# Performance work log

Hardware: AMD Instinct MI355X
Metric: run time of the kernel (lower is better)

The kernel has to match this reference:

```python
import jax, jax.numpy as jnp
import numpy as np

VOCAB_FACTORS = (16, 16, 16, 8)   # prod = 32768 = vocab_size
DIM_FACTORS = (4, 4, 4, 4)        # prod = 256   = projection_dim
RANKS = (1, 16, 16, 16, 1)        # tt_rank = 16
NUM_CORES = 4


def _core_shapes():
    return [(RANKS[k], VOCAB_FACTORS[k], DIM_FACTORS[k], RANKS[k + 1])
            for k in range(NUM_CORES)]


def _vocab_strides():
    # big-endian mixed-radix decomposition of a flat vocab index
    strides = []
    s = 1
    for n in reversed(VOCAB_FACTORS):
        strides.append(s)
        s *= n
    return tuple(reversed(strides))


def tt_lookup(cores, idx):
    """Reconstruct embedding rows from TT cores.
    cores[k]: [r_k, n_k, m_k, r_{k+1}];  idx: int array [...].
    Returns [..., prod(m_k)]."""
    flat = idx.reshape(-1)                                # [Bf]
    res = jnp.ones((flat.shape[0], 1, 1), dtype=cores[0].dtype)  # [Bf, M=1, r=1]
    for core, n, st in zip(cores, VOCAB_FACTORS, _vocab_strides()):
        digit = (flat // st) % n                          # [Bf]
        g = jnp.moveaxis(core[:, digit], 1, 0)            # [Bf, r, m, r']
        res = jnp.einsum('bMr,brms->bMms', res, g)        # [Bf, M, m, r']
        res = res.reshape(res.shape[0], -1, res.shape[-1])  # [Bf, M*m, r']
    D = res.shape[1]
    return res[..., 0].reshape(idx.shape + (D,))


def setup_inputs() -> dict:
    key = jax.random.key(0)
    ks = jax.random.split(key, 12)
    B, NEG, V = 8192, 20, int(np.prod(VOCAB_FACTORS))
    inp = {
        'center_words': jax.random.randint(ks[0], (B, 1), 0, V),
        'target_words': jax.random.randint(ks[1], (B, 1), 0, V),
        'negative_words': jax.random.randint(ks[2], (B, NEG), 0, V),
    }
    # embedding_v: glorot-style init spread over cores
    for k, shp in enumerate(_core_shapes()):
        glorot_std = float(np.sqrt(2.0 / (shp[0] * shp[1] + shp[2] * shp[3])))
        inp[f'v_core{k}'] = glorot_std * jax.random.normal(ks[3 + k], shp, dtype=jnp.float32)
    # embedding_u: stddev=1e-4 per the module
    for k, shp in enumerate(_core_shapes()):
        inp[f'u_core{k}'] = 1e-4 * jax.random.normal(ks[7 + k], shp, dtype=jnp.float32)
    return inp


def reference(center_words, target_words, negative_words,
              v_core0, v_core1, v_core2, v_core3,
              u_core0, u_core1, u_core2, u_core3):
    v_cores = (v_core0, v_core1, v_core2, v_core3)
    u_cores = (u_core0, u_core1, u_core2, u_core3)
    center_embeds = tt_lookup(v_cores, center_words)      # [B, 1, D]
    target_embeds = tt_lookup(u_cores, target_words)      # [B, 1, D]
    neg_embeds = -tt_lookup(u_cores, negative_words)      # [B, K, D]
    # target.bmm(center^T).squeeze(2) -> [B, 1]
    positive_score = jnp.einsum('bsd,btd->bs', target_embeds, center_embeds)
    # sum over negatives then view [B, 1]
    negative_score = jnp.sum(
        jnp.einsum('bkd,btd->bk', neg_embeds, center_embeds),
        axis=1, keepdims=True)                            # [B, 1]
    loss = jax.nn.log_sigmoid(positive_score) + jax.nn.log_sigmoid(negative_score)
    return -jnp.mean(loss)
```

## Files before the change

### kernel.cpp

```cpp
#include <hip/hip_runtime.h>
#include <hip/hip_bf16.h>

#define DEVINL __device__ __forceinline__

constexpr int NNEG   = 20;
constexpr int NBATCH = 8192;

constexpr int OFF_CORES = 0;
constexpr int N_CORE_ELEMS = 68608;
constexpr int OFF_H01V = 68608;
constexpr int OFF_H23V = 134144;
constexpr int OFF_H01U = 166912;
constexpr int OFF_H23U = 232448;
constexpr int OFF_PART = 265216;
constexpr int OFF_UTAB_F = 267264;
constexpr size_t WS_NEED_BYTES = (size_t)OFF_UTAB_F * 4 + (size_t)32768 * 256 * 2;

constexpr int CO_V0 = 0,     CO_V1 = 1024,  CO_V2 = 17408, CO_V3 = 33792;
constexpr int CO_U0 = 34304, CO_U1 = 35328, CO_U2 = 51712, CO_U3 = 68096;

DEVINL float bfbits_to_f32(unsigned short h) {
  unsigned int u = ((unsigned int)h) << 16;
  float f;
  __builtin_memcpy(&f, &u, sizeof(f));
  return f;
}

DEVINL unsigned short f32_to_bfbits(float f) {
  __hip_bfloat16 h = __float2bfloat16(f);
  unsigned short hb;
  __builtin_memcpy(&hb, &h, 2);
  return hb;
}

DEVINL bool sniff_is_f32(const void* probe) {
  const unsigned short* p = (const unsigned short*)probe;
  int insane = 0;
#pragma unroll 1
  for (int i = 0; i < 64; ++i) {
    unsigned short h = p[i];
    int e = (h >> 7) & 0xFF;
    if (h != 0 && (e < 90 || e > 140)) insane++;
  }
  return insane > 8;
}

__global__ void tt_convert(const void* v0, const void* v1, const void* v2, const void* v3,
                           const void* u0, const void* u1, const void* u2, const void* u3,
                           float* __restrict__ ws) {
  int t = blockIdx.x * 256 + threadIdx.x;
  if (t >= N_CORE_ELEMS) return;
  bool isF32 = sniff_is_f32(v1);
  const void* src;
  int local;
  if      (t < CO_V1) { src = v0; local = t; }
  else if (t < CO_V2) { src = v1; local = t - CO_V1; }
  else if (t < CO_V3) { src = v2; local = t - CO_V2; }
  else if (t < CO_U0) { src = v3; local = t - CO_V3; }
  else if (t < CO_U1) { src = u0; local = t - CO_U0; }
  else if (t < CO_U2) { src = u1; local = t - CO_U1; }
  else if (t < CO_U3) { src = u2; local = t - CO_U2; }
  else                { src = u3; local = t - CO_U3; }
  float val = isF32 ? ((const float*)src)[local]
                    : bfbits_to_f32(((const unsigned short*)src)[local]);
  ws[t] = val;
}

__global__ void tt_htables(float* __restrict__ ws) {
  int t = blockIdx.x * 256 + threadIdx.x;
  const float* cores = ws + OFF_CORES;
  bool isU = t >= 98304;
  int lt = isU ? t - 98304 : t;
  const float* c0 = cores + (isU ? CO_U0 : CO_V0);
  const float* c1 = cores + (isU ? CO_U1 : CO_V1);
  const float* c2 = cores + (isU ? CO_U2 : CO_V2);
  const float* c3 = cores + (isU ? CO_U3 : CO_V3);
  float* dst = ws + (isU ? OFF_H01U : OFF_H01V);

  if (lt < 65536) {
    int combo = lt >> 8, e = lt & 255;
    int d0 = combo >> 4, d1 = combo & 15;
    int M01 = e >> 4, r2 = e & 15;
    int m0 = M01 >> 2, m1 = M01 & 3;
    float s = 0.f;
#pragma unroll
    for (int r1 = 0; r1 < 16; ++r1)
      s = fmaf(c0[(d0 * 4 + m0) * 16 + r1], c1[((r1 * 16 + d1) * 4 + m1) * 16 + r2], s);
    dst[lt] = s;
  } else {
    int lt2 = lt - 65536;
    int combo = lt2 >> 8, e = lt2 & 255;
    int d2 = combo >> 3, d3 = combo & 7;
    int m23 = e >> 4, r2 = e & 15;
    int m2 = m23 >> 2, m3 = m23 & 3;
    float s = 0.f;
#pragma unroll
    for (int r3 = 0; r3 < 16; ++r3)
      s = fmaf(c2[((r2 * 16 + d2) * 4 + m2) * 16 + r3], c3[(r3 * 8 + d3) * 4 + m3], s);
    dst[65536 + lt2] = s;
  }
}

DEVINL float4 ld4(const float* p) { return *reinterpret_cast<const float4*>(p); }

DEVINL float logsigf(float x) {
  return fminf(x, 0.0f) - log1pf(expf(-fabsf(x)));
}

DEVINL void frag16(const float* __restrict__ A, const float* __restrict__ Bt,
                   int l, float e[4]) {
  const float* Ar = A + (l >> 2) * 16;
  const float* Br = Bt + (l & 3) * 64;
  float a[16], b[64];
#pragma unroll
  for (int i = 0; i < 4; ++i) *reinterpret_cast<float4*>(&a[4 * i]) = ld4(Ar + 4 * i);
#pragma unroll
  for (int i = 0; i < 16; ++i) *reinterpret_cast<float4*>(&b[4 * i]) = ld4(Br + 4 * i);
  e[0] = e[1] = e[2] = e[3] = 0.f;
#pragma unroll
  for (int r = 0; r < 16; ++r) {
#pragma unroll
    for (int j = 0; j < 4; ++j) e[j] = fmaf(a[r], b[j * 16 + r], e[j]);
  }
}

__global__ __launch_bounds__(256) void tt_utab(const float* __restrict__ ws,
                                               unsigned short* __restrict__ utab) {
  const int w    = blockIdx.x * 4 + (threadIdx.x >> 6);
  const int l    = threadIdx.x & 63;
  const int lo   = w & 127;
  const int hi0  = (w >> 7) * 8;

  const float* Bt = ws + OFF_H23U + lo * 256 + (l & 3) * 64;
  float b[64];
#pragma unroll
  for (int i = 0; i < 16; ++i) *reinterpret_cast<float4*>(&b[4 * i]) = ld4(Bt + 4 * i);

  const float* Abase = ws + OFF_H01U + (size_t)hi0 * 256 + (l >> 2) * 16;

#pragma unroll
  for (int rr = 0; rr < 8; rr += 2) {
    float a0[16], a1[16];
#pragma unroll
    for (int i = 0; i < 4; ++i) {
      *reinterpret_cast<float4*>(&a0[4 * i]) = ld4(Abase + rr * 256 + 4 * i);
      *reinterpret_cast<float4*>(&a1[4 * i]) = ld4(Abase + (rr + 1) * 256 + 4 * i);
    }
    float e0[4] = {0.f, 0.f, 0.f, 0.f}, e1[4] = {0.f, 0.f, 0.f, 0.f};
#pragma unroll
    for (int r = 0; r < 16; ++r) {
#pragma unroll
      for (int j = 0; j < 4; ++j) {
        e0[j] = fmaf(a0[r], b[j * 16 + r], e0[j]);
        e1[j] = fmaf(a1[r], b[j * 16 + r], e1[j]);
      }
    }
    const size_t v0 = (size_t)(hi0 + rr) * 128 + lo;
    const size_t v1 = v0 + 128;
    ushort4 o0, o1;
    o0.x = f32_to_bfbits(e0[0]); o0.y = f32_to_bfbits(e0[1]);
    o0.z = f32_to_bfbits(e0[2]); o0.w = f32_to_bfbits(e0[3]);
    o1.x = f32_to_bfbits(e1[0]); o1.y = f32_to_bfbits(e1[1]);
    o1.z = f32_to_bfbits(e1[2]); o1.w = f32_to_bfbits(e1[3]);
    *reinterpret_cast<ushort4*>(utab + v0 * 256 + l * 4) = o0;
    *reinterpret_cast<ushort4*>(utab + v1 * 256 + l * 4) = o1;
  }
}

__global__ __launch_bounds__(256) void tt_main_fast(
    const int* __restrict__ cw, const int* __restrict__ tw, const int* __restrict__ nw,
    const float* __restrict__ ws, const unsigned short* __restrict__ utab,
    float* __restrict__ partials) {
  const int lane = threadIdx.x & 63;
  const int wid  = threadIdx.x >> 6;
  const int b    = blockIdx.x * 4 + wid;

  const int ci = cw[b];
  const int ti = tw[b];
  const int myneg = nw[b * NNEG + (lane < NNEG ? lane : 0)];

  float c[4];
  frag16(ws + OFF_H01V + (ci >> 7) * 256, ws + OFF_H23V + (ci & 127) * 256, lane, c);

  float pos = 0.f, nacc = 0.f;
#pragma unroll
  for (int k = 0; k < 21; ++k) {
    const int idx = (k == 0) ? ti : __shfl(myneg, k - 1, 64);
    ushort4 uv = *reinterpret_cast<const ushort4*>(utab + (size_t)idx * 256 + lane * 4);
    float p = fmaf(bfbits_to_f32(uv.x), c[0],
              fmaf(bfbits_to_f32(uv.y), c[1],
              fmaf(bfbits_to_f32(uv.z), c[2],
                   bfbits_to_f32(uv.w) * c[3])));
    if (k == 0) pos = p; else nacc += p;
  }

#pragma unroll
  for (int off = 32; off > 0; off >>= 1) {
    pos  += __shfl_xor(pos, off, 64);
    nacc += __shfl_xor(nacc, off, 64);
  }

  __shared__ float sred[4];
  if (lane == 0) sred[wid] = -(logsigf(pos) + logsigf(-nacc));
  __syncthreads();
  if (threadIdx.x == 0)
    partials[blockIdx.x] = sred[0] + sred[1] + sred[2] + sred[3];
}

__global__ __launch_bounds__(256) void tt_sgns_main(
    const int* __restrict__ cw, const int* __restrict__ tw, const int* __restrict__ nw,
    const float* __restrict__ ws, float* __restrict__ partials) {
  const int lane = threadIdx.x & 63;
  const int wid  = threadIdx.x >> 6;
  const int b    = blockIdx.x * 4 + wid;

  const int ci = cw[b];
  const int ti = tw[b];
  const int myneg = nw[b * NNEG + (lane < NNEG ? lane : 0)];

  float c[4];
  frag16(ws + OFF_H01V + (ci >> 7) * 256, ws + OFF_H23V + (ci & 127) * 256, lane, c);

  float pos = 0.f, nacc = 0.f;
#pragma unroll 1
  for (int k = 0; k < 21; ++k) {
    const int idx = (k == 0) ? ti : __shfl(myneg, k - 1, 64);
    float e[4];
    frag16(ws + OFF_H01U + (idx >> 7) * 256, ws + OFF_H23U + (idx & 127) * 256, lane, e);
    float p = fmaf(e[0], c[0], fmaf(e[1], c[1], fmaf(e[2], c[2], e[3] * c[3])));
    if (k == 0) pos = p; else nacc += p;
  }

#pragma unroll
  for (int off = 32; off > 0; off >>= 1) {
    pos  += __shfl_xor(pos, off, 64);
    nacc += __shfl_xor(nacc, off, 64);
  }

  __shared__ float sred[4];
  if (lane == 0) sred[wid] = -(logsigf(pos) + logsigf(-nacc));
  __syncthreads();
  if (threadIdx.x == 0)
    partials[blockIdx.x] = sred[0] + sred[1] + sred[2] + sred[3];
}

__global__ void tt_reduce(const float* __restrict__ partials, void* __restrict__ out) {
  float s = 0.f;
  for (int i = threadIdx.x; i < 2048; i += 256) s += partials[i];
#pragma unroll
  for (int off = 32; off > 0; off >>= 1) s += __shfl_xor(s, off, 64);
  __shared__ float sr[4];
  int lane = threadIdx.x & 63, wid = threadIdx.x >> 6;
  if (lane == 0) sr[wid] = s;
  __syncthreads();
  if (threadIdx.x == 0) {
    float res = (sr[0] + sr[1] + sr[2] + sr[3]) * (1.0f / 8192.0f);
    unsigned short hb = f32_to_bfbits(res);
    unsigned int word = (((unsigned int)hb) << 16) | (unsigned int)hb;
    *(unsigned int*)out = word;
  }
}

extern "C" void kernel_launch(void* const* d_in, const int* in_sizes, int n_in,
                              void* d_out, int out_size, void* d_ws, size_t ws_size,
                              hipStream_t stream) {
  const int* cw = (const int*)d_in[0];
  const int* tw = (const int*)d_in[1];
  const int* nw = (const int*)d_in[2];
  float* ws = (float*)d_ws;

  tt_convert<<<(N_CORE_ELEMS + 255) / 256, 256, 0, stream>>>(
      d_in[3], d_in[4], d_in[5], d_in[6], d_in[7], d_in[8], d_in[9], d_in[10], ws);
  tt_htables<<<196608 / 256, 256, 0, stream>>>(ws);

  if (ws_size >= WS_NEED_BYTES) {
    unsigned short* utab = (unsigned short*)(ws + OFF_UTAB_F);
    tt_utab<<<1024, 256, 0, stream>>>(ws, utab);
    tt_main_fast<<<NBATCH / 4, 256, 0, stream>>>(cw, tw, nw, ws, utab, ws + OFF_PART);
  } else {
    tt_sgns_main<<<NBATCH / 4, 256, 0, stream>>>(cw, tw, nw, ws, ws + OFF_PART);
  }
  tt_reduce<<<1, 256, 0, stream>>>(ws + OFF_PART, d_out);
}
```

Measured before the change: 61.89 us.

## Fuse core conversion into htables, precompute center table, fold reduce into main

Merges the dtype-conversion kernel into the htables kernel, which now reads the raw cores directly with a per-block dtype sniff. Adds a full bf16 center-embedding table built alongside the u table, so the main kernel loads one row instead of running a per-sample 16-rank contraction. The final reduction now runs in the last block of the main kernel, chosen by an atomic counter, which removes the separate reduce launch. In exchange it writes an extra 16MB table covering the whole vocabulary even though only 8192 center rows are used, needs more workspace, and adds atomic traffic.

After: 120.3 us. 1.94x slower.

```diff
diff --git a/kernel.cpp b/kernel.cpp
--- a/kernel.cpp
+++ b/kernel.cpp
@@ -5,19 +5,19 @@
 
 constexpr int NNEG   = 20;
 constexpr int NBATCH = 8192;
-
-constexpr int OFF_CORES = 0;
-constexpr int N_CORE_ELEMS = 68608;
+constexpr int NMAIN_BLOCKS = NBATCH / 4;
+
 constexpr int OFF_H01V = 68608;
 constexpr int OFF_H23V = 134144;
 constexpr int OFF_H01U = 166912;
 constexpr int OFF_H23U = 232448;
 constexpr int OFF_PART = 265216;
-constexpr int OFF_UTAB_F = 267264;
-constexpr size_t WS_NEED_BYTES = (size_t)OFF_UTAB_F * 4 + (size_t)32768 * 256 * 2;
-
-constexpr int CO_V0 = 0,     CO_V1 = 1024,  CO_V2 = 17408, CO_V3 = 33792;
-constexpr int CO_U0 = 34304, CO_U1 = 35328, CO_U2 = 51712, CO_U3 = 68096;
+constexpr int OFF_CTR  = 267264;
+constexpr int OFF_UTAB_F = 267268;
+constexpr size_t UTAB_BYTES = (size_t)32768 * 256 * 2;
+constexpr size_t VTAB_BYTE_OFF = (size_t)OFF_UTAB_F * 4 + UTAB_BYTES;
+constexpr size_t WS_NEED_BYTES = VTAB_BYTE_OFF + UTAB_BYTES;
+constexpr size_t WS_NEED_FALLBACK = (size_t)(OFF_CTR + 4) * 4;
 
 DEVINL float bfbits_to_f32(unsigned short h) {
   unsigned int u = ((unsigned int)h) << 16;
@@ -31,6 +31,11 @@
   unsigned short hb;
   __builtin_memcpy(&hb, &h, 2);
   return hb;
+}
+
+DEVINL float ldconv(const void* s, int i, bool isF32) {
+  return isF32 ? ((const float*)s)[i]
+               : bfbits_to_f32(((const unsigned short*)s)[i]);
 }
 
 DEVINL bool sniff_is_f32(const void* probe) {
@@ -45,36 +50,24 @@
   return insane > 8;
 }
 
-__global__ void tt_convert(const void* v0, const void* v1, const void* v2, const void* v3,
-                           const void* u0, const void* u1, const void* u2, const void* u3,
-                           float* __restrict__ ws) {
+__global__ __launch_bounds__(256) void tt_htables(
+    const void* v0, const void* v1, const void* v2, const void* v3,
+    const void* u0, const void* u1, const void* u2, const void* u3,
+    float* __restrict__ ws) {
+  if (blockIdx.x == 0 && threadIdx.x == 0) *(int*)(ws + OFF_CTR) = 0;
+
+  __shared__ bool sIsF32;
+  if (threadIdx.x == 0) sIsF32 = sniff_is_f32(v1);
+  __syncthreads();
+  const bool isF32 = sIsF32;
+
   int t = blockIdx.x * 256 + threadIdx.x;
-  if (t >= N_CORE_ELEMS) return;
-  bool isF32 = sniff_is_f32(v1);
-  const void* src;
-  int local;
-  if      (t < CO_V1) { src = v0; local = t; }
-  else if (t < CO_V2) { src = v1; local = t - CO_V1; }
-  else if (t < CO_V3) { src = v2; local = t - CO_V2; }
-  else if (t < CO_U0) { src = v3; local = t - CO_V3; }
-  else if (t < CO_U1) { src = u0; local = t - CO_U0; }
-  else if (t < CO_U2) { src = u1; local = t - CO_U1; }
-  else if (t < CO_U3) { src = u2; local = t - CO_U2; }
-  else                { src = u3; local = t - CO_U3; }
-  float val = isF32 ? ((const float*)src)[local]
-                    : bfbits_to_f32(((const unsigned short*)src)[local]);
-  ws[t] = val;
-}
-
-__global__ void tt_htables(float* __restrict__ ws) {
-  int t = blockIdx.x * 256 + threadIdx.x;
-  const float* cores = ws + OFF_CORES;
   bool isU = t >= 98304;
   int lt = isU ? t - 98304 : t;
-  const float* c0 = cores + (isU ? CO_U0 : CO_V0);
-  const float* c1 = cores + (isU ? CO_U1 : CO_V1);
-  const float* c2 = cores + (isU ? CO_U2 : CO_V2);
-  const float* c3 = cores + (isU ? CO_U3 : CO_V3);
+  const void* c0 = isU ? u0 : v0;
+  const void* c1 = isU ? u1 : v1;
+  const void* c2 = isU ? u2 : v2;
+  const void* c3 = isU ? u3 : v3;
   float* dst = ws + (isU ? OFF_H01U : OFF_H01V);
 
   if (lt < 65536) {
@@ -85,7 +78,8 @@
     float s = 0.f;
 #pragma unroll
     for (int r1 = 0; r1 < 16; ++r1)
-      s = fmaf(c0[(d0 * 4 + m0) * 16 + r1], c1[((r1 * 16 + d1) * 4 + m1) * 16 + r2], s);
+      s = fmaf(ldconv(c0, (d0 * 4 + m0) * 16 + r1, isF32),
+               ldconv(c1, ((r1 * 16 + d1) * 4 + m1) * 16 + r2, isF32), s);
     dst[lt] = s;
   } else {
     int lt2 = lt - 65536;
@@ -96,7 +90,8 @@
     float s = 0.f;
 #pragma unroll
     for (int r3 = 0; r3 < 16; ++r3)
-      s = fmaf(c2[((r2 * 16 + d2) * 4 + m2) * 16 + r3], c3[(r3 * 8 + d3) * 4 + m3], s);
+      s = fmaf(ldconv(c2, ((r2 * 16 + d2) * 4 + m2) * 16 + r3, isF32),
+               ldconv(c3, (r3 * 8 + d3) * 4 + m3, isF32), s);
     dst[65536 + lt2] = s;
   }
 }
@@ -107,36 +102,25 @@
   return fminf(x, 0.0f) - log1pf(expf(-fabsf(x)));
 }
 
-DEVINL void frag16(const float* __restrict__ A, const float* __restrict__ Bt,
-                   int l, float e[4]) {
-  const float* Ar = A + (l >> 2) * 16;
-  const float* Br = Bt + (l & 3) * 64;
-  float a[16], b[64];
-#pragma unroll
-  for (int i = 0; i < 4; ++i) *reinterpret_cast<float4*>(&a[4 * i]) = ld4(Ar + 4 * i);
-#pragma unroll
-  for (int i = 0; i < 16; ++i) *reinterpret_cast<float4*>(&b[4 * i]) = ld4(Br + 4 * i);
-  e[0] = e[1] = e[2] = e[3] = 0.f;
-#pragma unroll
-  for (int r = 0; r < 16; ++r) {
-#pragma unroll
-    for (int j = 0; j < 4; ++j) e[j] = fmaf(a[r], b[j * 16 + r], e[j]);
-  }
-}
-
-__global__ __launch_bounds__(256) void tt_utab(const float* __restrict__ ws,
-                                               unsigned short* __restrict__ utab) {
-  const int w    = blockIdx.x * 4 + (threadIdx.x >> 6);
+__global__ __launch_bounds__(256) void tt_tabs(const float* __restrict__ ws,
+                                               unsigned short* __restrict__ utab,
+                                               unsigned short* __restrict__ vtab) {
+  const bool isV = blockIdx.x >= 1024;
+  const int w    = (blockIdx.x & 1023) * 4 + (threadIdx.x >> 6);
   const int l    = threadIdx.x & 63;
   const int lo   = w & 127;
   const int hi0  = (w >> 7) * 8;
 
-  const float* Bt = ws + OFF_H23U + lo * 256 + (l & 3) * 64;
+  const float* H01 = ws + (isV ? OFF_H01V : OFF_H01U);
+  const float* H23 = ws + (isV ? OFF_H23V : OFF_H23U);
+  unsigned short* dst = isV ? vtab : utab;
+
+  const float* Bt = H23 + lo * 256 + (l & 3) * 64;
   float b[64];
 #pragma unroll
   for (int i = 0; i < 16; ++i) *reinterpret_cast<float4*>(&b[4 * i]) = ld4(Bt + 4 * i);
 
-  const float* Abase = ws + OFF_H01U + (size_t)hi0 * 256 + (l >> 2) * 16;
+  const float* Abase = H01 + (size_t)hi0 * 256 + (l >> 2) * 16;
 
 #pragma unroll
   for (int rr = 0; rr < 8; rr += 2) {
@@ -155,42 +139,56 @@
         e1[j] = fmaf(a1[r], b[j * 16 + r], e1[j]);
       }
     }
-    const size_t v0 = (size_t)(hi0 + rr) * 128 + lo;
-    const size_t v1 = v0 + 128;
+    const size_t v0i = (size_t)(hi0 + rr) * 128 + lo;
+    const size_t v1i = v0i + 128;
     ushort4 o0, o1;
     o0.x = f32_to_bfbits(e0[0]); o0.y = f32_to_bfbits(e0[1]);
     o0.z = f32_to_bfbits(e0[2]); o0.w = f32_to_bfbits(e0[3]);
     o1.x = f32_to_bfbits(e1[0]); o1.y = f32_to_bfbits(e1[1]);
     o1.z = f32_to_bfbits(e1[2]); o1.w = f32_to_bfbits(e1[3]);
-    *reinterpret_cast<ushort4*>(utab + v0 * 256 + l * 4) = o0;
-    *reinterpret_cast<ushort4*>(utab + v1 * 256 + l * 4) = o1;
-  }
-}
-
-__global__ __launch_bounds__(256) void tt_main_fast(
+    *reinterpret_cast<ushort4*>(dst + v0i * 256 + l * 4) = o0;
+    *reinterpret_cast<ushort4*>(dst + v1i * 256 + l * 4) = o1;
+  }
+}
+
+DEVINL float dot4_bf(ushort4 uv, const float c[4]) {
+  return fmaf(bfbits_to_f32(uv.x), c[0],
+         fmaf(bfbits_to_f32(uv.y), c[1],
+         fmaf(bfbits_to_f32(uv.z), c[2],
+              bfbits_to_f32(uv.w) * c[3])));
+}
+
+__global__ __launch_bounds__(256) void tt_main2(
     const int* __restrict__ cw, const int* __restrict__ tw, const int* __restrict__ nw,
-    const float* __restrict__ ws, const unsigned short* __restrict__ utab,
-    float* __restrict__ partials) {
+    const unsigned short* __restrict__ utab, const unsigned short* __restrict__ vtab,
+    float* __restrict__ partials, int* __restrict__ ctr, void* __restrict__ out) {
   const int lane = threadIdx.x & 63;
   const int wid  = threadIdx.x >> 6;
   const int b    = blockIdx.x * 4 + wid;
 
+  __shared__ int sidx[4][24];
+  __shared__ float sred[4];
+  __shared__ float sr2[4];
+  __shared__ int elected;
+
+  if (lane < 21)
+    sidx[wid][lane] = (lane == 0) ? tw[b] : nw[b * NNEG + lane - 1];
   const int ci = cw[b];
-  const int ti = tw[b];
-  const int myneg = nw[b * NNEG + (lane < NNEG ? lane : 0)];
 
   float c[4];
-  frag16(ws + OFF_H01V + (ci >> 7) * 256, ws + OFF_H23V + (ci & 127) * 256, lane, c);
+  {
+    ushort4 cv = *reinterpret_cast<const ushort4*>(vtab + (size_t)ci * 256 + lane * 4);
+    c[0] = bfbits_to_f32(cv.x); c[1] = bfbits_to_f32(cv.y);
+    c[2] = bfbits_to_f32(cv.z); c[3] = bfbits_to_f32(cv.w);
+  }
+  __syncthreads();
 
   float pos = 0.f, nacc = 0.f;
 #pragma unroll
   for (int k = 0; k < 21; ++k) {
-    const int idx = (k == 0) ? ti : __shfl(myneg, k - 1, 64);
+    const int idx = sidx[wid][k];
     ushort4 uv = *reinterpret_cast<const ushort4*>(utab + (size_t)idx * 256 + lane * 4);
-    float p = fmaf(bfbits_to_f32(uv.x), c[0],
-              fmaf(bfbits_to_f32(uv.y), c[1],
-              fmaf(bfbits_to_f32(uv.z), c[2],
-                   bfbits_to_f32(uv.w) * c[3])));
+    float p = dot4_bf(uv, c);
     if (k == 0) pos = p; else nacc += p;
   }
 
@@ -200,11 +198,49 @@
     nacc += __shfl_xor(nacc, off, 64);
   }
 
-  __shared__ float sred[4];
   if (lane == 0) sred[wid] = -(logsigf(pos) + logsigf(-nacc));
   __syncthreads();
-  if (threadIdx.x == 0)
-    partials[blockIdx.x] = sred[0] + sred[1] + sred[2] + sred[3];
+
+  if (threadIdx.x == 0) {
+    float p = sred[0] + sred[1] + sred[2] + sred[3];
+    __hip_atomic_store(&partials[blockIdx.x], p, __ATOMIC_RELAXED, __HIP_MEMORY_SCOPE_AGENT);
+    int old = __hip_atomic_fetch_add(ctr, 1, __ATOMIC_ACQ_REL, __HIP_MEMORY_SCOPE_AGENT);
+    elected = (old == (int)gridDim.x - 1) ? 1 : 0;
+  }
+  __syncthreads();
+
+  if (elected) {
+    float s = 0.f;
+    for (int i = threadIdx.x; i < NMAIN_BLOCKS; i += 256)
+      s += __hip_atomic_load(&partials[i], __ATOMIC_RELAXED, __HIP_MEMORY_SCOPE_AGENT);
+#pragma unroll
+    for (int off = 32; off > 0; off >>= 1) s += __shfl_xor(s, off, 64);
+    if (lane == 0) sr2[wid] = s;
+    __syncthreads();
+    if (threadIdx.x == 0) {
+      float res = (sr2[0] + sr2[1] + sr2[2] + sr2[3]) * (1.0f / 8192.0f);
+      unsigned short hb = f32_to_bfbits(res);
+      unsigned int word = (((unsigned int)hb) << 16) | (unsigned int)hb;
+      *(unsigned int*)out = word;
+    }
+  }
+}
+
+DEVINL void frag16(const float* __restrict__ A, const float* __restrict__ Bt,
+                   int l, float e[4]) {
+  const float* Ar = A + (l >> 2) * 16;
+  const float* Br = Bt + (l & 3) * 64;
+  float a[16], bb[64];
+#pragma unroll
+  for (int i = 0; i < 4; ++i) *reinterpret_cast<float4*>(&a[4 * i]) = ld4(Ar + 4 * i);
+#pragma unroll
+  for (int i = 0; i < 16; ++i) *reinterpret_cast<float4*>(&bb[4 * i]) = ld4(Br + 4 * i);
+  e[0] = e[1] = e[2] = e[3] = 0.f;
+#pragma unroll
+  for (int r = 0; r < 16; ++r) {
+#pragma unroll
+    for (int j = 0; j < 4; ++j) e[j] = fmaf(a[r], bb[j * 16 + r], e[j]);
+  }
 }
 
 __global__ __launch_bounds__(256) void tt_sgns_main(
@@ -246,7 +282,7 @@
 
 __global__ void tt_reduce(const float* __restrict__ partials, void* __restrict__ out) {
   float s = 0.f;
-  for (int i = threadIdx.x; i < 2048; i += 256) s += partials[i];
+  for (int i = threadIdx.x; i < NMAIN_BLOCKS; i += 256) s += partials[i];
 #pragma unroll
   for (int off = 32; off > 0; off >>= 1) s += __shfl_xor(s, off, 64);
   __shared__ float sr[4];
@@ -269,16 +305,17 @@
   const int* nw = (const int*)d_in[2];
   float* ws = (float*)d_ws;
 
-  tt_convert<<<(N_CORE_ELEMS + 255) / 256, 256, 0, stream>>>(
+  tt_htables<<<768, 256, 0, stream>>>(
       d_in[3], d_in[4], d_in[5], d_in[6], d_in[7], d_in[8], d_in[9], d_in[10], ws);
-  tt_htables<<<196608 / 256, 256, 0, stream>>>(ws);
 
   if (ws_size >= WS_NEED_BYTES) {
     unsigned short* utab = (unsigned short*)(ws + OFF_UTAB_F);
-    tt_utab<<<1024, 256, 0, stream>>>(ws, utab);
-    tt_main_fast<<<NBATCH / 4, 256, 0, stream>>>(cw, tw, nw, ws, utab, ws + OFF_PART);
+    unsigned short* vtab = (unsigned short*)((char*)d_ws + VTAB_BYTE_OFF);
+    tt_tabs<<<2048, 256, 0, stream>>>(ws, utab, vtab);
+    tt_main2<<<NMAIN_BLOCKS, 256, 0, stream>>>(
+        cw, tw, nw, utab, vtab, ws + OFF_PART, (int*)(ws + OFF_CTR), d_out);
   } else {
-    tt_sgns_main<<<NBATCH / 4, 256, 0, stream>>>(cw, tw, nw, ws, ws + OFF_PART);
-  }
-  tt_reduce<<<1, 256, 0, stream>>>(ws + OFF_PART, d_out);
-}
+    tt_sgns_main<<<NMAIN_BLOCKS, 256, 0, stream>>>(cw, tw, nw, ws, ws + OFF_PART);
+    tt_reduce<<<1, 256, 0, stream>>>(ws + OFF_PART, d_out);
+  }
+}
```
